# Optimization experiments

Measured on AMD Instinct MI355X. Metric: run time of the kernel, lower is better.

## Reference

```python
import jax, jax.numpy as jnp
import numpy as np

D_MODEL = 768
N_HEADS = 12
D_K = 768
D_V = 768
SEQ = 2048
BATCH = 2


def setup_inputs() -> dict:
    key = jax.random.key(0)
    ks = jax.random.split(key, 9)
    s = 0.02
    return {
        "x": jax.random.normal(ks[0], (SEQ, BATCH, D_MODEL), dtype=jnp.float32),
        "Wq": jax.random.normal(ks[1], (D_MODEL, D_K), dtype=jnp.float32) * s,
        "bq": jnp.zeros((D_K,), dtype=jnp.float32),
        "Wk": jax.random.normal(ks[2], (D_MODEL, D_K), dtype=jnp.float32) * s,
        "bk": jnp.zeros((D_K,), dtype=jnp.float32),
        "Wv": jax.random.normal(ks[3], (D_MODEL, D_V), dtype=jnp.float32) * s,
        "bv": jnp.zeros((D_V,), dtype=jnp.float32),
        "Wo": jax.random.normal(ks[4], (D_V, D_MODEL), dtype=jnp.float32) * s,
        "bo": jnp.zeros((D_MODEL,), dtype=jnp.float32),
    }


def reference(x, Wq, bq, Wk, bk, Wv, bv, Wo, bo):
    # x: (S, B, D)
    S, B, D = x.shape
    H = N_HEADS
    hk = D_K // H
    hv = D_V // H
    q = (x @ Wq + bq).reshape(S, B, H, hk)
    k = (x @ Wk + bk).reshape(S, B, H, hk)
    v = (x @ Wv + bv).reshape(S, B, H, hv)
    scale = 1.0 / np.sqrt(hk).astype(np.float32)
    # scores: (B, H, S_q, S_k)
    att = jnp.einsum("sbhd,tbhd->bhst", q, k) * scale
    causal = jnp.triu(jnp.ones((S, S), dtype=bool), k=1)  # True above diagonal
    att = jnp.where(causal, jnp.float32(-jnp.inf), att)
    att = jax.nn.softmax(att, axis=-1)
    y = jnp.einsum("bhst,tbhd->sbhd", att, v).reshape(S, B, D_V)
    return y @ Wo + bo  # (S, B, D)
```

## Files before the change

### kernel.cpp

```cpp
#include <hip/hip_runtime.h>

typedef __attribute__((ext_vector_type(8))) short short8;
typedef __attribute__((ext_vector_type(4))) short s16x4;
typedef __attribute__((ext_vector_type(4))) float f32x4;

#define NHEADS 12
#define SEQLEN 2048
#define HEADD  64
#define DMODEL 768

__device__ __forceinline__ short cvtbf(float f) {
  unsigned u = __builtin_bit_cast(unsigned, f);
  u += 0x7fffu + ((u >> 16) & 1u);
  return (short)(u >> 16);
}

__device__ __forceinline__ void gload16(const void* g, void* l) {
  __builtin_amdgcn_global_load_lds((const __attribute__((address_space(1))) void*)g,
                                   (__attribute__((address_space(3))) void*)l, 16, 0, 0);
}

__device__ __forceinline__ void ds_write_hi16(short* p, float v) {
  asm volatile("ds_write_b16_d16_hi %0, %1"
               : : "v"((__attribute__((address_space(3))) short*)p), "v"(v) : "memory");
}

__global__ void prep_kernel(const float* __restrict__ x, short* __restrict__ xb,
                            const float* __restrict__ w0, const float* __restrict__ w1,
                            const float* __restrict__ w2, const float* __restrict__ w3,
                            short* __restrict__ wt, short* __restrict__ wot) {
  __shared__ float t[32][33];
  const int tid = threadIdx.x;
  if (blockIdx.x < 1536) {
    int i = blockIdx.x * 256 + tid;
    const float* p = x + (size_t)i * 8;
    short8 v;
#pragma unroll
    for (int j = 0; j < 8; ++j) v[j] = cvtbf(p[j]);
    *(short8*)(xb + (size_t)i * 8) = v;
    return;
  }
  int bx = blockIdx.x - 1536;
  int bz = bx / 576, rem = bx - bz * 576;
  int bxx = rem % 24, byy = rem / 24;
  const float* W = bz == 0 ? w0 : bz == 1 ? w1 : bz == 2 ? w2 : w3;
  short* O = bz < 3 ? wt + (size_t)bz * (768 * 768) : wot;
  int tx = tid & 31, ty = tid >> 5;
  int n0 = bxx * 32, k0 = byy * 32;
#pragma unroll
  for (int j = 0; j < 4; ++j)
    t[ty + j * 8][tx] = W[(k0 + ty + j * 8) * 768 + n0 + tx];
  __syncthreads();
#pragma unroll
  for (int j = 0; j < 4; ++j)
    O[(n0 + ty + j * 8) * 768 + k0 + tx] = cvtbf(t[tx][ty + j * 8]);
}

template <bool DBUF>
__device__ __forceinline__ void gemm_core128(const short* __restrict__ A,
                                             const short* __restrict__ Bt,
                                             short* sA, short* sB,
                                             int bm, int bn, f32x4 acc[4][4]) {
  const int tid = threadIdx.x;
  const int w = tid >> 6, lane = tid & 63;
  const int quad = lane >> 4, l16 = lane & 15;
  const int wm = (w & 1) * 64, wn = (w >> 1) * 64;

  int gA[4], gB[4], lbase[4];
#pragma unroll
  for (int j = 0; j < 4; ++j) {
    int slot = j * 256 + w * 64 + lane;
    int r = slot >> 3, c = (slot & 7) ^ (r & 7);
    gA[j] = (bm * 128 + r) * 768 + c * 8;
    gB[j] = (bn * 128 + r) * 768 + c * 8;
    lbase[j] = (j * 256 + w * 64) * 8;
  }

  if (DBUF) {
#pragma unroll
    for (int j = 0; j < 4; ++j) {
      gload16(A + gA[j], sA + lbase[j]);
      gload16(Bt + gB[j], sB + lbase[j]);
    }
    int pb = 0;
    for (int kt = 0; kt < 12; ++kt) {
      __syncthreads();
      if (kt + 1 < 12) {
        int o = (pb ^ 1) * 8192;
#pragma unroll
        for (int j = 0; j < 4; ++j) {
          gload16(A + gA[j] + (kt + 1) * 64, sA + o + lbase[j]);
          gload16(Bt + gB[j] + (kt + 1) * 64, sB + o + lbase[j]);
        }
      }
      const short* pa = sA + pb * 8192;
      const short* pbv = sB + pb * 8192;
#pragma unroll
      for (int ks = 0; ks < 2; ++ks) {
        int cp = (ks * 4 + quad) ^ (l16 & 7);
        short8 a[4], b[4];
#pragma unroll
        for (int mt = 0; mt < 4; ++mt)
          a[mt] = *(const short8*)(pa + (wm + mt * 16 + l16) * 64 + cp * 8);
#pragma unroll
        for (int nt = 0; nt < 4; ++nt)
          b[nt] = *(const short8*)(pbv + (wn + nt * 16 + l16) * 64 + cp * 8);
#pragma unroll
        for (int mt = 0; mt < 4; ++mt)
#pragma unroll
          for (int nt = 0; nt < 4; ++nt)
            acc[mt][nt] = __builtin_amdgcn_mfma_f32_16x16x32_bf16(a[mt], b[nt], acc[mt][nt], 0, 0, 0);
      }
      pb ^= 1;
    }
  } else {
    for (int kt = 0; kt < 12; ++kt) {
      __syncthreads();
#pragma unroll
      for (int j = 0; j < 4; ++j) {
        gload16(A + gA[j] + kt * 64, sA + lbase[j]);
        gload16(Bt + gB[j] + kt * 64, sB + lbase[j]);
      }
      __syncthreads();
#pragma unroll
      for (int ks = 0; ks < 2; ++ks) {
        int cp = (ks * 4 + quad) ^ (l16 & 7);
        short8 a[4], b[4];
#pragma unroll
        for (int mt = 0; mt < 4; ++mt)
          a[mt] = *(const short8*)(sA + (wm + mt * 16 + l16) * 64 + cp * 8);
#pragma unroll
        for (int nt = 0; nt < 4; ++nt)
          b[nt] = *(const short8*)(sB + (wn + nt * 16 + l16) * 64 + cp * 8);
#pragma unroll
        for (int mt = 0; mt < 4; ++mt)
#pragma unroll
          for (int nt = 0; nt < 4; ++nt)
            acc[mt][nt] = __builtin_amdgcn_mfma_f32_16x16x32_bf16(a[mt], b[nt], acc[mt][nt], 0, 0, 0);
      }
    }
  }
}

__global__ __launch_bounds__(256, 3) void qkv_gemm(
    const short* __restrict__ A, const short* __restrict__ Bt,
    const float* __restrict__ bq, const float* __restrict__ bk, const float* __restrict__ bv,
    short* __restrict__ oq, short* __restrict__ ok, short* __restrict__ ov) {
  __shared__ short sA[128 * 64];
  __shared__ short sB[128 * 64];
  f32x4 acc[4][4];
  const f32x4 z4 = {0.f, 0.f, 0.f, 0.f};
#pragma unroll
  for (int mt = 0; mt < 4; ++mt)
#pragma unroll
    for (int nt = 0; nt < 4; ++nt) acc[mt][nt] = z4;

  const int bm = blockIdx.x, bn = blockIdx.y;
  gemm_core128<false>(A, Bt, sA, sB, bm, bn, acc);

  const int seg = bn / 6, bn_l = bn % 6;
  const float* bias = seg == 0 ? bq : seg == 1 ? bk : bv;
  short* outp = seg == 0 ? oq : seg == 1 ? ok : ov;

  const int tid = threadIdx.x;
  const int w = tid >> 6, lane = tid & 63;
  const int quad = lane >> 4, l16 = lane & 15;
  const int wm = (w & 1) * 64, wn = (w >> 1) * 64;

#pragma unroll
  for (int nt = 0; nt < 4; ++nt) {
    int n = bn_l * 128 + wn + nt * 16 + l16;
    float bval = bias[n];
    int h = n >> 6, d = n & 63;
#pragma unroll
    for (int mt = 0; mt < 4; ++mt) {
      int rowb = wm + mt * 16 + quad * 4;
#pragma unroll
      for (int r = 0; r < 4; ++r) {
        int m = bm * 128 + rowb + r;
        int s = m >> 1, b = m & 1;
        float v = acc[mt][nt][r] + bval;
        if (seg == 0) v *= 0.1803368801f;
        if (seg < 2)
          outp[((b * NHEADS + h) * SEQLEN + s) * HEADD + d] = cvtbf(v);
        else
          outp[((b * NHEADS + h) * HEADD + d) * SEQLEN + s] = cvtbf(v);
      }
    }
  }
}

#define AE(qi, ts, nt) ((qi) | ((ts) << 8) | ((nt) << 16))
__device__ const int ATTN_TAB[80] = {
  AE(31,0,8), AE(31,8,8), AE(31,16,8), AE(31,24,8),
  AE(30,0,8), AE(30,8,8), AE(30,16,8),
  AE(29,0,8), AE(29,8,8), AE(29,16,8),
  AE(28,0,8), AE(28,8,8), AE(28,16,8),
  AE(27,0,8), AE(27,8,8), AE(27,16,8),
  AE(26,0,8), AE(26,8,8), AE(26,16,8),
  AE(25,0,8), AE(25,8,8), AE(25,16,8),
  AE(24,0,8), AE(24,8,8), AE(24,16,8),
  AE(23,0,8), AE(23,8,8), AE(23,16,8),
  AE(22,0,8), AE(22,8,8),
  AE(21,0,8), AE(21,8,8),
  AE(20,0,8), AE(20,8,8),
  AE(19,0,8), AE(19,8,8),
  AE(18,0,8), AE(18,8,8),
  AE(17,0,8), AE(17,8,8),
  AE(16,0,8), AE(16,8,8),
  AE(15,0,8), AE(15,8,8),
  AE(14,0,8), AE(13,0,8), AE(12,0,8), AE(11,0,8),
  AE(10,0,8), AE(9,0,8),  AE(8,0,8),  AE(7,0,8),
  AE(30,24,7), AE(22,16,7), AE(14,8,7), AE(6,0,7),
  AE(29,24,6), AE(21,16,6), AE(13,8,6), AE(5,0,6),
  AE(28,24,5), AE(20,16,5), AE(12,8,5), AE(4,0,5),
  AE(27,24,4), AE(19,16,4), AE(11,8,4), AE(3,0,4),
  AE(26,24,3), AE(18,16,3), AE(10,8,3), AE(2,0,3),
  AE(25,24,2), AE(17,16,2), AE(9,8,2),  AE(1,0,2),
  AE(24,24,1), AE(16,16,1), AE(8,8,1),  AE(0,0,1),
};
__device__ const int PBASE[32] = {
  0,0,0,0,0,0,0,0,
  0,2,4,6,8,10,12,14,
  16,19,22,25,28,31,34,37,
  40,44,48,52,56,60,64,68};

__global__ __launch_bounds__(256, 4) void attn_kernel(
    const short* __restrict__ Q, const short* __restrict__ K,
    const short* __restrict__ Vt, short* __restrict__ Y,
    float* __restrict__ Of, float* __restrict__ lf) {
  __shared__ short sK[2][64 * 64];
  __shared__ short sV[2][64 * 64];
  __shared__ short sP[64 * 64];
  const int tid = threadIdx.x;
  const int w = tid >> 6, lane = tid & 63;
  const int quad = lane >> 4, l16 = lane & 15;
  const int e = ATTN_TAB[blockIdx.x / 24];
  const int bh = blockIdx.x % 24;
  const int qi = e & 255, ts = (e >> 8) & 255, ntl = e >> 16;
  const int q0 = qi << 6;
  const short* Qb = Q + (size_t)bh * (SEQLEN * HEADD);
  const short* Kb = K + (size_t)bh * (SEQLEN * HEADD);
  const short* Vb = Vt + (size_t)bh * (SEQLEN * HEADD);

  short8 aq[2];
#pragma unroll
  for (int ks = 0; ks < 2; ++ks)
    aq[ks] = *(const short8*)(Qb + (q0 + w * 16 + l16) * 64 + ks * 32 + quad * 8);

  const short8 bones = {0x3F80, 0x3F80, 0x3F80, 0x3F80, 0x3F80, 0x3F80, 0x3F80, 0x3F80};
  f32x4 acc_o[4], acc_l;
  const f32x4 z4 = {0.f, 0.f, 0.f, 0.f};
#pragma unroll
  for (int nt = 0; nt < 4; ++nt) acc_o[nt] = z4;
  acc_l = z4;

  int gK[2], gV[2], lbase[2];
#pragma unroll
  for (int j = 0; j < 2; ++j) {
    int slot = j * 256 + w * 64 + lane;
    int r = slot >> 3, c = (slot & 7) ^ (r & 7);
    gK[j] = r * 64 + c * 8;
    gV[j] = r * 2048 + c * 8;
    lbase[j] = (j * 256 + w * 64) * 8;
  }

  const int qrow = q0 + w * 16 + quad * 4;
  const int tend = ts + ntl;

#pragma unroll
  for (int j = 0; j < 2; ++j) {
    gload16(Kb + (ts << 6) * 64 + gK[j], &sK[0][lbase[j]]);
    gload16(Vb + (ts << 6) + gV[j], &sV[0][lbase[j]]);
  }

  int pb = 0;
  for (int it = ts; it < tend; ++it) {
    __syncthreads();
    if (it + 1 < tend) {
      const int t1 = (it + 1) << 6;
#pragma unroll
      for (int j = 0; j < 2; ++j) {
        gload16(Kb + t1 * 64 + gK[j], &sK[pb ^ 1][lbase[j]]);
        gload16(Vb + t1 + gV[j], &sV[pb ^ 1][lbase[j]]);
      }
    }
    const short* sk = sK[pb];
    const short* sv = sV[pb];

    f32x4 sc[4];
#pragma unroll
    for (int nt = 0; nt < 4; ++nt) sc[nt] = z4;
    __builtin_amdgcn_s_setprio(1);
#pragma unroll
    for (int ks = 0; ks < 2; ++ks) {
      int cp = (ks * 4 + quad) ^ (l16 & 7);
#pragma unroll
      for (int nt = 0; nt < 4; ++nt) {
        short8 bk = *(const short8*)(sk + (nt * 16 + l16) * 64 + cp * 8);
        sc[nt] = __builtin_amdgcn_mfma_f32_16x16x32_bf16(aq[ks], bk, sc[nt], 0, 0, 0);
      }
    }
    __builtin_amdgcn_s_setprio(0);

    if (it == qi) {
      const int t0 = it << 6;
#pragma unroll
      for (int nt = 0; nt < 4; ++nt)
#pragma unroll
        for (int r = 0; r < 4; ++r) {
          int t = t0 + nt * 16 + l16;
          if (t > qrow + r) sc[nt][r] = -1e30f;
        }
    }

#pragma unroll
    for (int nt = 0; nt < 4; ++nt)
#pragma unroll
      for (int r = 0; r < 4; ++r) {
        float p = __builtin_amdgcn_exp2f(sc[nt][r]);
        int rq = w * 16 + quad * 4 + r;
        int t = nt * 16 + l16;
        int c = t >> 3;
        ds_write_hi16(&sP[rq * 64 + ((c ^ (rq & 7)) * 8 + (t & 7))], p);
      }

    __builtin_amdgcn_s_setprio(1);
#pragma unroll
    for (int kst = 0; kst < 2; ++kst) {
      int rq = w * 16 + l16;
      int cpa = (kst * 4 + quad) ^ (rq & 7);
      short8 ap = *(const short8*)(sP + rq * 64 + cpa * 8);
      acc_l = __builtin_amdgcn_mfma_f32_16x16x32_bf16(ap, bones, acc_l, 0, 0, 0);
#pragma unroll
      for (int nt = 0; nt < 4; ++nt) {
        int row = nt * 16 + l16;
        int cv = (kst * 4 + quad) ^ (row & 7);
        short8 bv = *(const short8*)(sv + row * 64 + cv * 8);
        acc_o[nt] = __builtin_amdgcn_mfma_f32_16x16x32_bf16(ap, bv, acc_o[nt], 0, 0, 0);
      }
    }
    __builtin_amdgcn_s_setprio(0);
    pb ^= 1;
  }

  if (qi < 8) {
    const int b = bh / NHEADS, h = bh % NHEADS;
#pragma unroll
    for (int r = 0; r < 4; ++r) {
      float rl = __builtin_amdgcn_rcpf(acc_l[r]);
      int srow = q0 + w * 16 + quad * 4 + r;
#pragma unroll
      for (int nt = 0; nt < 4; ++nt)
        Y[(srow * 2 + b) * DMODEL + h * 64 + nt * 16 + l16] = cvtbf(acc_o[nt][r] * rl);
    }
  } else {
    const int slot = bh * 72 + PBASE[qi] + (ts >> 3);
    float* Ob = Of + (size_t)slot * 4096;
#pragma unroll
    for (int r = 0; r < 4; ++r) {
      int row = w * 16 + quad * 4 + r;
#pragma unroll
      for (int nt = 0; nt < 4; ++nt)
        Ob[row * 64 + nt * 16 + l16] = acc_o[nt][r];
      if (l16 == 0) lf[slot * 64 + row] = acc_l[r];
    }
  }
}

__global__ void attn_merge(const float* __restrict__ Of, const float* __restrict__ lf,
                           short* __restrict__ Y) {
  const int bh = blockIdx.x % 24, qi = 8 + blockIdx.x / 24;
  const int nch = (qi >> 3) + 1;
  const int base = bh * 72 + PBASE[qi];
  const float* O0 = Of + (size_t)base * 4096;
  const float* L0 = lf + base * 64;
  const int b = bh / NHEADS, h = bh % NHEADS;
  const int tid = threadIdx.x;
#pragma unroll
  for (int j = 0; j < 4; ++j) {
    int i4 = j * 256 + tid;
    int row = i4 >> 4, col4 = (i4 & 15) * 4;
    f32x4 o = *(const f32x4*)(O0 + (size_t)i4 * 4);
    float l = L0[row];
    for (int c = 1; c < nch; ++c) {
      o += *(const f32x4*)(O0 + (size_t)c * 4096 + (size_t)i4 * 4);
      l += L0[c * 64 + row];
    }
    float rl = __builtin_amdgcn_rcpf(l);
    s16x4 y;
#pragma unroll
    for (int k = 0; k < 4; ++k) y[k] = cvtbf(o[k] * rl);
    int srow = qi * 64 + row;
    *(s16x4*)(Y + (size_t)(srow * 2 + b) * DMODEL + h * 64 + col4) = y;
  }
}

__global__ __launch_bounds__(256, 2) void oproj_gemm(
    const short* __restrict__ A, const short* __restrict__ Bt,
    const float* __restrict__ bo, float* __restrict__ out) {
  __shared__ short sA[2 * 128 * 64];
  __shared__ short sB[2 * 128 * 64];
  f32x4 acc[4][4];
  const f32x4 z4 = {0.f, 0.f, 0.f, 0.f};
#pragma unroll
  for (int mt = 0; mt < 4; ++mt)
#pragma unroll
    for (int nt = 0; nt < 4; ++nt) acc[mt][nt] = z4;

  const int bm = blockIdx.x, bn = blockIdx.y;
  gemm_core128<true>(A, Bt, sA, sB, bm, bn, acc);

  const int tid = threadIdx.x;
  const int w = tid >> 6, lane = tid & 63;
  const int quad = lane >> 4, l16 = lane & 15;
  const int wm = (w & 1) * 64, wn = (w >> 1) * 64;

#pragma unroll
  for (int nt = 0; nt < 4; ++nt) {
    int n = bn * 128 + wn + nt * 16 + l16;
    float bval = bo[n];
#pragma unroll
    for (int mt = 0; mt < 4; ++mt) {
      int rowb = wm + mt * 16 + quad * 4;
#pragma unroll
      for (int r = 0; r < 4; ++r) {
        int m = bm * 128 + rowb + r;
        out[(size_t)m * 768 + n] = acc[mt][nt][r] + bval;
      }
    }
  }
}

extern "C" void kernel_launch(void* const* d_in, const int* in_sizes, int n_in,
                              void* d_out, int out_size, void* d_ws, size_t ws_size,
                              hipStream_t stream) {
  const float* x  = (const float*)d_in[0];
  const float* Wq = (const float*)d_in[1];
  const float* bq = (const float*)d_in[2];
  const float* Wk = (const float*)d_in[3];
  const float* bk = (const float*)d_in[4];
  const float* Wv = (const float*)d_in[5];
  const float* bv = (const float*)d_in[6];
  const float* Wo = (const float*)d_in[7];
  const float* bo = (const float*)d_in[8];
  float* out = (float*)d_out;

  short* ws  = (short*)d_ws;
  short* xb  = ws;
  short* wt  = ws + 3145728;
  short* wot = ws + 4915200;
  short* qw  = ws + 5505024;
  short* kw  = ws + 8650752;
  short* vw  = ws + 11796480;
  short* yw  = ws + 14942208;
  float* Of  = (float*)(ws + 18087936);
  float* lf  = Of + 7077888;

  prep_kernel<<<3840, 256, 0, stream>>>(x, xb, Wq, Wk, Wv, Wo, wt, wot);
  qkv_gemm<<<dim3(32, 18), 256, 0, stream>>>(xb, wt, bq, bk, bv, qw, kw, vw);
  attn_kernel<<<1920, 256, 0, stream>>>(qw, kw, vw, yw, Of, lf);
  attn_merge<<<576, 256, 0, stream>>>(Of, lf, yw);
  oproj_gemm<<<dim3(32, 6), 256, 0, stream>>>(yw, wot, bo, out);
}
```

Measured before the change: 154.7 us.

## Use two waves per attention block, each handling 32 query rows

```diff
diff --git a/kernel.cpp b/kernel.cpp
--- a/kernel.cpp
+++ b/kernel.cpp
@@ -225,7 +225,7 @@
   16,19,22,25,28,31,34,37,
   40,44,48,52,56,60,64,68};
 
-__global__ __launch_bounds__(256, 4) void attn_kernel(
+__global__ __launch_bounds__(128, 2) void attn_kernel(
     const short* __restrict__ Q, const short* __restrict__ K,
     const short* __restrict__ Vt, short* __restrict__ Y,
     float* __restrict__ Of, float* __restrict__ lf) {
@@ -243,33 +243,37 @@
   const short* Kb = K + (size_t)bh * (SEQLEN * HEADD);
   const short* Vb = Vt + (size_t)bh * (SEQLEN * HEADD);
 
-  short8 aq[2];
-#pragma unroll
-  for (int ks = 0; ks < 2; ++ks)
-    aq[ks] = *(const short8*)(Qb + (q0 + w * 16 + l16) * 64 + ks * 32 + quad * 8);
+  short8 aq[2][2];
+#pragma unroll
+  for (int m = 0; m < 2; ++m)
+#pragma unroll
+    for (int ks = 0; ks < 2; ++ks)
+      aq[m][ks] = *(const short8*)(Qb + (q0 + w * 32 + m * 16 + l16) * 64 + ks * 32 + quad * 8);
 
   const short8 bones = {0x3F80, 0x3F80, 0x3F80, 0x3F80, 0x3F80, 0x3F80, 0x3F80, 0x3F80};
-  f32x4 acc_o[4], acc_l;
+  f32x4 acc_o[2][4], acc_l[2];
   const f32x4 z4 = {0.f, 0.f, 0.f, 0.f};
 #pragma unroll
-  for (int nt = 0; nt < 4; ++nt) acc_o[nt] = z4;
-  acc_l = z4;
-
-  int gK[2], gV[2], lbase[2];
-#pragma unroll
-  for (int j = 0; j < 2; ++j) {
-    int slot = j * 256 + w * 64 + lane;
+  for (int m = 0; m < 2; ++m) {
+#pragma unroll
+    for (int nt = 0; nt < 4; ++nt) acc_o[m][nt] = z4;
+    acc_l[m] = z4;
+  }
+
+  int gK[4], gV[4], lbase[4];
+#pragma unroll
+  for (int j = 0; j < 4; ++j) {
+    int slot = j * 128 + w * 64 + lane;
     int r = slot >> 3, c = (slot & 7) ^ (r & 7);
     gK[j] = r * 64 + c * 8;
     gV[j] = r * 2048 + c * 8;
-    lbase[j] = (j * 256 + w * 64) * 8;
-  }
-
-  const int qrow = q0 + w * 16 + quad * 4;
+    lbase[j] = (j * 128 + w * 64) * 8;
+  }
+
   const int tend = ts + ntl;
 
 #pragma unroll
-  for (int j = 0; j < 2; ++j) {
+  for (int j = 0; j < 4; ++j) {
     gload16(Kb + (ts << 6) * 64 + gK[j], &sK[0][lbase[j]]);
     gload16(Vb + (ts << 6) + gV[j], &sV[0][lbase[j]]);
   }
@@ -280,7 +284,7 @@
     if (it + 1 < tend) {
       const int t1 = (it + 1) << 6;
 #pragma unroll
-      for (int j = 0; j < 2; ++j) {
+      for (int j = 0; j < 4; ++j) {
         gload16(Kb + t1 * 64 + gK[j], &sK[pb ^ 1][lbase[j]]);
         gload16(Vb + t1 + gV[j], &sV[pb ^ 1][lbase[j]]);
       }
@@ -288,9 +292,11 @@
     const short* sk = sK[pb];
     const short* sv = sV[pb];
 
-    f32x4 sc[4];
-#pragma unroll
-    for (int nt = 0; nt < 4; ++nt) sc[nt] = z4;
+    f32x4 sc[2][4];
+#pragma unroll
+    for (int m = 0; m < 2; ++m)
+#pragma unroll
+      for (int nt = 0; nt < 4; ++nt) sc[m][nt] = z4;
     __builtin_amdgcn_s_setprio(1);
 #pragma unroll
     for (int ks = 0; ks < 2; ++ks) {
@@ -298,7 +304,9 @@
 #pragma unroll
       for (int nt = 0; nt < 4; ++nt) {
         short8 bk = *(const short8*)(sk + (nt * 16 + l16) * 64 + cp * 8);
-        sc[nt] = __builtin_amdgcn_mfma_f32_16x16x32_bf16(aq[ks], bk, sc[nt], 0, 0, 0);
+#pragma unroll
+        for (int m = 0; m < 2; ++m)
+          sc[m][nt] = __builtin_amdgcn_mfma_f32_16x16x32_bf16(aq[m][ks], bk, sc[m][nt], 0, 0, 0);
       }
     }
     __builtin_amdgcn_s_setprio(0);
@@ -306,38 +314,50 @@
     if (it == qi) {
       const int t0 = it << 6;
 #pragma unroll
+      for (int m = 0; m < 2; ++m) {
+        int qrow = q0 + w * 32 + m * 16 + quad * 4;
+#pragma unroll
+        for (int nt = 0; nt < 4; ++nt)
+#pragma unroll
+          for (int r = 0; r < 4; ++r) {
+            int t = t0 + nt * 16 + l16;
+            if (t > qrow + r) sc[m][nt][r] = -1e30f;
+          }
+      }
+    }
+
+#pragma unroll
+    for (int m = 0; m < 2; ++m)
+#pragma unroll
       for (int nt = 0; nt < 4; ++nt)
 #pragma unroll
         for (int r = 0; r < 4; ++r) {
-          int t = t0 + nt * 16 + l16;
-          if (t > qrow + r) sc[nt][r] = -1e30f;
+          float p = __builtin_amdgcn_exp2f(sc[m][nt][r]);
+          int rq = w * 32 + m * 16 + quad * 4 + r;
+          int t = nt * 16 + l16;
+          int c = t >> 3;
+          ds_write_hi16(&sP[rq * 64 + ((c ^ (rq & 7)) * 8 + (t & 7))], p);
         }
-    }
-
-#pragma unroll
-    for (int nt = 0; nt < 4; ++nt)
-#pragma unroll
-      for (int r = 0; r < 4; ++r) {
-        float p = __builtin_amdgcn_exp2f(sc[nt][r]);
-        int rq = w * 16 + quad * 4 + r;
-        int t = nt * 16 + l16;
-        int c = t >> 3;
-        ds_write_hi16(&sP[rq * 64 + ((c ^ (rq & 7)) * 8 + (t & 7))], p);
-      }
 
     __builtin_amdgcn_s_setprio(1);
 #pragma unroll
     for (int kst = 0; kst < 2; ++kst) {
-      int rq = w * 16 + l16;
-      int cpa = (kst * 4 + quad) ^ (rq & 7);
-      short8 ap = *(const short8*)(sP + rq * 64 + cpa * 8);
-      acc_l = __builtin_amdgcn_mfma_f32_16x16x32_bf16(ap, bones, acc_l, 0, 0, 0);
+      short8 ap[2];
+#pragma unroll
+      for (int m = 0; m < 2; ++m) {
+        int rq = w * 32 + m * 16 + l16;
+        int cpa = (kst * 4 + quad) ^ (rq & 7);
+        ap[m] = *(const short8*)(sP + rq * 64 + cpa * 8);
+        acc_l[m] = __builtin_amdgcn_mfma_f32_16x16x32_bf16(ap[m], bones, acc_l[m], 0, 0, 0);
+      }
 #pragma unroll
       for (int nt = 0; nt < 4; ++nt) {
         int row = nt * 16 + l16;
         int cv = (kst * 4 + quad) ^ (row & 7);
         short8 bv = *(const short8*)(sv + row * 64 + cv * 8);
-        acc_o[nt] = __builtin_amdgcn_mfma_f32_16x16x32_bf16(ap, bv, acc_o[nt], 0, 0, 0);
+#pragma unroll
+        for (int m = 0; m < 2; ++m)
+          acc_o[m][nt] = __builtin_amdgcn_mfma_f32_16x16x32_bf16(ap[m], bv, acc_o[m][nt], 0, 0, 0);
       }
     }
     __builtin_amdgcn_s_setprio(0);
@@ -347,24 +367,28 @@
   if (qi < 8) {
     const int b = bh / NHEADS, h = bh % NHEADS;
 #pragma unroll
-    for (int r = 0; r < 4; ++r) {
-      float rl = __builtin_amdgcn_rcpf(acc_l[r]);
-      int srow = q0 + w * 16 + quad * 4 + r;
-#pragma unroll
-      for (int nt = 0; nt < 4; ++nt)
-        Y[(srow * 2 + b) * DMODEL + h * 64 + nt * 16 + l16] = cvtbf(acc_o[nt][r] * rl);
-    }
+    for (int m = 0; m < 2; ++m)
+#pragma unroll
+      for (int r = 0; r < 4; ++r) {
+        float rl = __builtin_amdgcn_rcpf(acc_l[m][r]);
+        int srow = q0 + w * 32 + m * 16 + quad * 4 + r;
+#pragma unroll
+        for (int nt = 0; nt < 4; ++nt)
+          Y[(srow * 2 + b) * DMODEL + h * 64 + nt * 16 + l16] = cvtbf(acc_o[m][nt][r] * rl);
+      }
   } else {
     const int slot = bh * 72 + PBASE[qi] + (ts >> 3);
     float* Ob = Of + (size_t)slot * 4096;
 #pragma unroll
-    for (int r = 0; r < 4; ++r) {
-      int row = w * 16 + quad * 4 + r;
-#pragma unroll
-      for (int nt = 0; nt < 4; ++nt)
-        Ob[row * 64 + nt * 16 + l16] = acc_o[nt][r];
-      if (l16 == 0) lf[slot * 64 + row] = acc_l[r];
-    }
+    for (int m = 0; m < 2; ++m)
+#pragma unroll
+      for (int r = 0; r < 4; ++r) {
+        int row = w * 32 + m * 16 + quad * 4 + r;
+#pragma unroll
+        for (int nt = 0; nt < 4; ++nt)
+          Ob[row * 64 + nt * 16 + l16] = acc_o[m][nt][r];
+        if (l16 == 0) lf[slot * 64 + row] = acc_l[m][r];
+      }
   }
 }
 
@@ -459,7 +483,7 @@
 
   prep_kernel<<<3840, 256, 0, stream>>>(x, xb, Wq, Wk, Wv, Wo, wt, wot);
   qkv_gemm<<<dim3(32, 18), 256, 0, stream>>>(xb, wt, bq, bk, bv, qw, kw, vw);
-  attn_kernel<<<1920, 256, 0, stream>>>(qw, kw, vw, yw, Of, lf);
+  attn_kernel<<<1920, 128, 0, stream>>>(qw, kw, vw, yw, Of, lf);
   attn_merge<<<576, 256, 0, stream>>>(Of, lf, yw);
   oproj_gemm<<<dim3(32, 6), 256, 0, stream>>>(yw, wot, bo, out);
 }
```

Result: no change. 157.2 us (+1.6%).
